# Performance work log

Measured on AMD Instinct MI355X. Metric: run time of the kernel, lower is better.

The kernel has to match this reference:

```python
import jax, jax.numpy as jnp
import numpy as np

B, S, K, N = 4, 2048, 4096, 16384  # batch, seq, in_features, out_features


def setup_inputs() -> dict:
    key = jax.random.key(0)
    k1, k2, k3, k4 = jax.random.split(key, 4)
    x = jax.random.normal(k1, (B, S, K), dtype=jnp.float32)
    # symmetric int8 quantized weights, stored as int32 (values in int8 range)
    W_q = jax.random.randint(k2, (N, K), -128, 128, dtype=jnp.int32)
    # per-output-channel scales (positive, divisor in original code)
    scales = jax.random.uniform(k3, (N,), dtype=jnp.float32, minval=0.5, maxval=2.0)
    bias = jax.random.normal(k4, (N,), dtype=jnp.float32)
    return {"x": x, "W_q": W_q, "scales": scales, "bias": bias}


def reference(x, W_q, scales, bias):
    # out = (x @ W_q.T) / scales + bias   (dequantize-by-division, per out channel)
    Wf = W_q.astype(x.dtype)                       # [N, K]
    lead = x.shape[:-1]
    out = jnp.einsum('tk,nk->tn', x.reshape(-1, x.shape[-1]), Wf)  # [B*S, N]
    out = out / scales[None, :] + bias[None, :]
    return out.reshape(lead + (W_q.shape[0],))
```

## Files before the change

kernel.cpp:

```cpp
#include <hip/hip_runtime.h>
#include <hip/hip_bf16.h>
#include <stdint.h>
#include <stddef.h>

#define M_DIM 8192
#define K_DIM 4096
#define N_DIM 16384

typedef __attribute__((ext_vector_type(8))) short short8;
typedef __attribute__((ext_vector_type(4))) float f32x4;

__device__ __forceinline__ unsigned short f2bf(float f) {
    union { float f; uint32_t u; } c; c.f = f;
    uint32_t u = c.u;
    return (unsigned short)((u + 0x7FFFu + ((u >> 16) & 1u)) >> 16);
}


__global__ __launch_bounds__(256) void conv_x_kernel(const float* __restrict__ x,
                                                     unsigned short* __restrict__ out) {
    size_t i = ((size_t)blockIdx.x * 256 + threadIdx.x) * 8;
    const float4* p = (const float4*)(x + i);
    float4 u = p[0], v = p[1];
    short8 h;
    h[0] = (short)f2bf(u.x); h[1] = (short)f2bf(u.y);
    h[2] = (short)f2bf(u.z); h[3] = (short)f2bf(u.w);
    h[4] = (short)f2bf(v.x); h[5] = (short)f2bf(v.y);
    h[6] = (short)f2bf(v.z); h[7] = (short)f2bf(v.w);
    *(short8*)(out + i) = h;
}

__global__ __launch_bounds__(256) void conv_w_kernel(const int* __restrict__ w,
                                                     unsigned short* __restrict__ out) {
    size_t i = ((size_t)blockIdx.x * 256 + threadIdx.x) * 8;
    const int4* p = (const int4*)(w + i);
    int4 u = p[0], v = p[1];
    short8 h;
    h[0] = (short)f2bf((float)u.x); h[1] = (short)f2bf((float)u.y);
    h[2] = (short)f2bf((float)u.z); h[3] = (short)f2bf((float)u.w);
    h[4] = (short)f2bf((float)v.x); h[5] = (short)f2bf((float)v.y);
    h[6] = (short)f2bf((float)v.z); h[7] = (short)f2bf((float)v.w);
    *(short8*)(out + i) = h;
}


__device__ __forceinline__ void gld_lds16(const void* g, void* l) {
    __builtin_amdgcn_global_load_lds(
        (__attribute__((address_space(1))) void*)(g),
        (__attribute__((address_space(3))) void*)(l),
        16, 0, 0);
}


__global__ __launch_bounds__(256) void gemm_a_kernel(
    const unsigned short* __restrict__ A,
    const unsigned short* __restrict__ Bm,
    const float* __restrict__ scales,
    const float* __restrict__ bias,
    float* __restrict__ C) {
    __shared__ unsigned short As[128 * 64];
    __shared__ unsigned short Bs[128 * 64];

    const int tid = threadIdx.x;
    const int m0 = blockIdx.y * 128;
    const int n0 = blockIdx.x * 128;
    const int lane = tid & 63;
    const int wv = tid >> 6;
    const int wm = (wv & 1) * 64;
    const int wn = (wv >> 1) * 64;
    const int lm = lane & 15;
    const int lk = (lane >> 4) * 8;

    f32x4 acc[4][4] = {};

    for (int kt = 0; kt < K_DIM / 64; ++kt) {
        const int k0 = kt * 64;
#pragma unroll
        for (int i = 0; i < 4; ++i) {
            int c = tid + i * 256;
            int row = c >> 3, col = (c & 7) * 8;
            gld_lds16(A + (size_t)(m0 + row) * K_DIM + k0 + col, (char*)As + c * 16);
        }
#pragma unroll
        for (int i = 0; i < 4; ++i) {
            int c = tid + i * 256;
            int row = c >> 3, col = (c & 7) * 8;
            gld_lds16(Bm + (size_t)(n0 + row) * K_DIM + k0 + col, (char*)Bs + c * 16);
        }
        __syncthreads();

#pragma unroll
        for (int kk = 0; kk < 64; kk += 32) {
            short8 af[4], bfr[4];
#pragma unroll
            for (int im = 0; im < 4; ++im)
                af[im] = *(const short8*)&As[(wm + im * 16 + lm) * 64 + kk + lk];
#pragma unroll
            for (int jn = 0; jn < 4; ++jn)
                bfr[jn] = *(const short8*)&Bs[(wn + jn * 16 + lm) * 64 + kk + lk];
#pragma unroll
            for (int im = 0; im < 4; ++im)
#pragma unroll
                for (int jn = 0; jn < 4; ++jn)
                    acc[im][jn] = __builtin_amdgcn_mfma_f32_16x16x32_bf16(
                        af[im], bfr[jn], acc[im][jn], 0, 0, 0);
        }
        __syncthreads();
    }

#pragma unroll
    for (int jn = 0; jn < 4; ++jn) {
        const int col = n0 + wn + jn * 16 + lm;
        const float inv = 1.0f / scales[col];
        const float bb = bias[col];
#pragma unroll
        for (int im = 0; im < 4; ++im) {
            const int r0 = m0 + wm + im * 16 + (lane >> 4) * 4;
#pragma unroll
            for (int r = 0; r < 4; ++r)
                C[(size_t)(r0 + r) * N_DIM + col] = acc[im][jn][r] * inv + bb;
        }
    }
}


__global__ __launch_bounds__(256) void gemm_b_kernel(
    const float* __restrict__ X,
    const int* __restrict__ W,
    const float* __restrict__ scales,
    const float* __restrict__ bias,
    float* __restrict__ C) {
    __shared__ unsigned short As[128 * 64];
    __shared__ unsigned short Bs[128 * 64];

    const int tid = threadIdx.x;
    const int m0 = blockIdx.y * 128;
    const int n0 = blockIdx.x * 128;
    const int lane = tid & 63;
    const int wv = tid >> 6;
    const int wm = (wv & 1) * 64;
    const int wn = (wv >> 1) * 64;
    const int lm = lane & 15;
    const int lk = (lane >> 4) * 8;

    f32x4 acc[4][4] = {};

    for (int kt = 0; kt < K_DIM / 64; ++kt) {
        const int k0 = kt * 64;
#pragma unroll
        for (int i = 0; i < 4; ++i) {
            int c = tid + i * 256;
            int row = c >> 3, col = (c & 7) * 8;
            const float* p = X + (size_t)(m0 + row) * K_DIM + k0 + col;
            float4 u = *(const float4*)p;
            float4 v = *(const float4*)(p + 4);
            short8 h;
            h[0] = (short)f2bf(u.x); h[1] = (short)f2bf(u.y);
            h[2] = (short)f2bf(u.z); h[3] = (short)f2bf(u.w);
            h[4] = (short)f2bf(v.x); h[5] = (short)f2bf(v.y);
            h[6] = (short)f2bf(v.z); h[7] = (short)f2bf(v.w);
            *(short8*)&As[(size_t)c * 8] = h;
        }
#pragma unroll
        for (int i = 0; i < 4; ++i) {
            int c = tid + i * 256;
            int row = c >> 3, col = (c & 7) * 8;
            const int* p = W + (size_t)(n0 + row) * K_DIM + k0 + col;
            int4 u = *(const int4*)p;
            int4 v = *(const int4*)(p + 4);
            short8 h;
            h[0] = (short)f2bf((float)u.x); h[1] = (short)f2bf((float)u.y);
            h[2] = (short)f2bf((float)u.z); h[3] = (short)f2bf((float)u.w);
            h[4] = (short)f2bf((float)v.x); h[5] = (short)f2bf((float)v.y);
            h[6] = (short)f2bf((float)v.z); h[7] = (short)f2bf((float)v.w);
            *(short8*)&Bs[(size_t)c * 8] = h;
        }
        __syncthreads();

#pragma unroll
        for (int kk = 0; kk < 64; kk += 32) {
            short8 af[4], bfr[4];
#pragma unroll
            for (int im = 0; im < 4; ++im)
                af[im] = *(const short8*)&As[(wm + im * 16 + lm) * 64 + kk + lk];
#pragma unroll
            for (int jn = 0; jn < 4; ++jn)
                bfr[jn] = *(const short8*)&Bs[(wn + jn * 16 + lm) * 64 + kk + lk];
#pragma unroll
            for (int im = 0; im < 4; ++im)
#pragma unroll
                for (int jn = 0; jn < 4; ++jn)
                    acc[im][jn] = __builtin_amdgcn_mfma_f32_16x16x32_bf16(
                        af[im], bfr[jn], acc[im][jn], 0, 0, 0);
        }
        __syncthreads();
    }

#pragma unroll
    for (int jn = 0; jn < 4; ++jn) {
        const int col = n0 + wn + jn * 16 + lm;
        const float inv = 1.0f / scales[col];
        const float bb = bias[col];
#pragma unroll
        for (int im = 0; im < 4; ++im) {
            const int r0 = m0 + wm + im * 16 + (lane >> 4) * 4;
#pragma unroll
            for (int r = 0; r < 4; ++r)
                C[(size_t)(r0 + r) * N_DIM + col] = acc[im][jn][r] * inv + bb;
        }
    }
}


extern "C" void kernel_launch(void* const* d_in, const int* in_sizes, int n_in,
                              void* d_out, int out_size, void* d_ws, size_t ws_size,
                              hipStream_t stream) {
    const float* x      = (const float*)d_in[0];
    const int*   wq     = (const int*)d_in[1];
    const float* scales = (const float*)d_in[2];
    const float* bias   = (const float*)d_in[3];
    float* out = (float*)d_out;

    const size_t x_elems = (size_t)M_DIM * K_DIM;
    const size_t w_elems = (size_t)N_DIM * K_DIM;
    const size_t need = (x_elems + w_elems) * sizeof(unsigned short);

    dim3 grid(N_DIM / 128, M_DIM / 128);

    if (ws_size >= need) {
        unsigned short* xbf = (unsigned short*)d_ws;
        unsigned short* wbf = xbf + x_elems;
        conv_x_kernel<<<(int)(x_elems / (256 * 8)), 256, 0, stream>>>(x, xbf);
        conv_w_kernel<<<(int)(w_elems / (256 * 8)), 256, 0, stream>>>(wq, wbf);
        gemm_a_kernel<<<grid, 256, 0, stream>>>(xbf, wbf, scales, bias, out);
    } else {
        gemm_b_kernel<<<grid, 256, 0, stream>>>(x, wq, scales, bias, out);
    }
}
```

Measured before the change: 2.320 ms.

## Rewrite bf16 GEMM as 256x256 tile, 8-wave, double-buffered pipelined kernel

Replaces the 128x128 single-buffered GEMM with a 256x256-tile, 512-thread kernel. It double-buffers LDS, uses XOR-swizzled layouts to avoid bank conflicts, and interleaves async global-to-LDS loads of the next K tile with four MFMA phases. The phases are separated by barriers and raised wave priority, and tiles are remapped for L2 locality. This targets global-load latency stalls and LDS conflicts. In exchange it needs 128KB of LDS and many accumulator registers, and relies on careful vmcnt accounting that is fragile.

```diff
diff --git a/kernel.cpp b/kernel.cpp
--- a/kernel.cpp
+++ b/kernel.cpp
@@ -6,6 +6,7 @@
 #define M_DIM 8192
 #define K_DIM 4096
 #define N_DIM 16384
+#define NT (K_DIM / 64)
 
 typedef __attribute__((ext_vector_type(8))) short short8;
 typedef __attribute__((ext_vector_type(4))) float f32x4;
@@ -51,74 +52,172 @@
         16, 0, 0);
 }
 
-
-__global__ __launch_bounds__(256) void gemm_a_kernel(
+__device__ __forceinline__ void stage_half(const unsigned short* __restrict__ src,
+                                           unsigned short* lbase, int tid) {
+#pragma unroll
+    for (int i = 0; i < 2; ++i) {
+        int c = tid + i * 512;
+        int row = c >> 3;
+        int col = ((c & 7) ^ (row & 7)) << 3;
+        gld_lds16(src + (size_t)row * K_DIM + col, (char*)lbase + (size_t)c * 16);
+    }
+}
+
+__device__ __forceinline__ short8 lds_frag(const unsigned short* base, int r, int kc) {
+    return *(const short8*)(base + r * 64 + ((kc ^ (r & 7)) << 3));
+}
+
+#define BAR()                                \
+    do {                                     \
+        asm volatile("" ::: "memory");       \
+        __builtin_amdgcn_s_barrier();        \
+        asm volatile("" ::: "memory");       \
+    } while (0)
+#define LGKM0() asm volatile("s_waitcnt lgkmcnt(0)" ::: "memory")
+
+
+__global__ __launch_bounds__(512, 2) void gemm_a_kernel(
     const unsigned short* __restrict__ A,
     const unsigned short* __restrict__ Bm,
     const float* __restrict__ scales,
     const float* __restrict__ bias,
     float* __restrict__ C) {
-    __shared__ unsigned short As[128 * 64];
-    __shared__ unsigned short Bs[128 * 64];
+    __shared__ unsigned short As[2][256 * 64];
+    __shared__ unsigned short Bs[2][256 * 64];
 
     const int tid = threadIdx.x;
-    const int m0 = blockIdx.y * 128;
-    const int n0 = blockIdx.x * 128;
     const int lane = tid & 63;
     const int wv = tid >> 6;
-    const int wm = (wv & 1) * 64;
+    const int wm = (wv & 1) * 128;
     const int wn = (wv >> 1) * 64;
     const int lm = lane & 15;
-    const int lk = (lane >> 4) * 8;
-
-    f32x4 acc[4][4] = {};
-
-    for (int kt = 0; kt < K_DIM / 64; ++kt) {
-        const int k0 = kt * 64;
-#pragma unroll
-        for (int i = 0; i < 4; ++i) {
-            int c = tid + i * 256;
-            int row = c >> 3, col = (c & 7) * 8;
-            gld_lds16(A + (size_t)(m0 + row) * K_DIM + k0 + col, (char*)As + c * 16);
-        }
-#pragma unroll
-        for (int i = 0; i < 4; ++i) {
-            int c = tid + i * 256;
-            int row = c >> 3, col = (c & 7) * 8;
-            gld_lds16(Bm + (size_t)(n0 + row) * K_DIM + k0 + col, (char*)Bs + c * 16);
-        }
-        __syncthreads();
-
-#pragma unroll
-        for (int kk = 0; kk < 64; kk += 32) {
-            short8 af[4], bfr[4];
-#pragma unroll
-            for (int im = 0; im < 4; ++im)
-                af[im] = *(const short8*)&As[(wm + im * 16 + lm) * 64 + kk + lk];
-#pragma unroll
-            for (int jn = 0; jn < 4; ++jn)
-                bfr[jn] = *(const short8*)&Bs[(wn + jn * 16 + lm) * 64 + kk + lk];
-#pragma unroll
-            for (int im = 0; im < 4; ++im)
-#pragma unroll
-                for (int jn = 0; jn < 4; ++jn)
+    const int kseg = lane >> 4;
+
+    const int bid = blockIdx.x;
+    const int tm = (bid & 7) * 4 + ((bid >> 3) & 3);
+    const int tn = bid >> 5;
+    const int m0 = tm * 256, n0 = tn * 256;
+
+    const unsigned short* Ab = A + (size_t)m0 * K_DIM;
+    const unsigned short* Bb = Bm + (size_t)n0 * K_DIM;
+
+    f32x4 acc[8][4] = {};
+    short8 a[4][2], bA[2][2], bB[2][2];
+
+    stage_half(Ab,                            &As[0][0],        tid);
+    stage_half(Ab + (size_t)128 * K_DIM,      &As[0][128 * 64], tid);
+    stage_half(Bb,                            &Bs[0][0],        tid);
+    stage_half(Bb + (size_t)128 * K_DIM,      &Bs[0][128 * 64], tid);
+    stage_half(Bb + 64,                       &Bs[1][0],        tid);
+    stage_half(Bb + (size_t)128 * K_DIM + 64, &Bs[1][128 * 64], tid);
+    asm volatile("s_waitcnt vmcnt(4)" ::: "memory");
+    BAR();
+
+    for (int t = 0; t < NT; ++t) {
+        const int cb = t & 1;
+        const unsigned short* Ac = &As[cb][0];
+        const unsigned short* Bc = &Bs[cb][0];
+        unsigned short* Anx = &As[cb ^ 1][0];
+        unsigned short* Bnx = &Bs[cb][0];
+        const size_t kA = (size_t)((t + 1 < NT) ? t + 1 : NT - 1) * 64;
+        const size_t kB = (size_t)((t + 2 < NT) ? t + 2 : NT - 1) * 64;
+
+#pragma unroll
+        for (int im = 0; im < 4; ++im)
+#pragma unroll
+            for (int kx = 0; kx < 2; ++kx)
+                a[im][kx] = lds_frag(Ac, wm + im * 16 + lm, kx * 4 + kseg);
+#pragma unroll
+        for (int jn = 0; jn < 2; ++jn)
+#pragma unroll
+            for (int kx = 0; kx < 2; ++kx)
+                bA[jn][kx] = lds_frag(Bc, wn + jn * 16 + lm, kx * 4 + kseg);
+        stage_half(Ab + kA, Anx, tid);
+        BAR();
+        LGKM0();
+        __builtin_amdgcn_s_setprio(1);
+#pragma unroll
+        for (int im = 0; im < 4; ++im)
+#pragma unroll
+            for (int jn = 0; jn < 2; ++jn)
+#pragma unroll
+                for (int kx = 0; kx < 2; ++kx)
                     acc[im][jn] = __builtin_amdgcn_mfma_f32_16x16x32_bf16(
-                        af[im], bfr[jn], acc[im][jn], 0, 0, 0);
-        }
-        __syncthreads();
-    }
+                        a[im][kx], bA[jn][kx], acc[im][jn], 0, 0, 0);
+        __builtin_amdgcn_s_setprio(0);
+        BAR();
+
+#pragma unroll
+        for (int jn = 0; jn < 2; ++jn)
+#pragma unroll
+            for (int kx = 0; kx < 2; ++kx)
+                bB[jn][kx] = lds_frag(Bc, wn + (jn + 2) * 16 + lm, kx * 4 + kseg);
+        stage_half(Ab + (size_t)128 * K_DIM + kA, Anx + 128 * 64, tid);
+        BAR();
+        LGKM0();
+        __builtin_amdgcn_s_setprio(1);
+#pragma unroll
+        for (int im = 0; im < 4; ++im)
+#pragma unroll
+            for (int jn = 0; jn < 2; ++jn)
+#pragma unroll
+                for (int kx = 0; kx < 2; ++kx)
+                    acc[im][jn + 2] = __builtin_amdgcn_mfma_f32_16x16x32_bf16(
+                        a[im][kx], bB[jn][kx], acc[im][jn + 2], 0, 0, 0);
+        __builtin_amdgcn_s_setprio(0);
+        BAR();
+
+#pragma unroll
+        for (int im = 0; im < 4; ++im)
+#pragma unroll
+            for (int kx = 0; kx < 2; ++kx)
+                a[im][kx] = lds_frag(Ac, wm + (im + 4) * 16 + lm, kx * 4 + kseg);
+        stage_half(Bb + kB, Bnx, tid);
+        BAR();
+        LGKM0();
+        __builtin_amdgcn_s_setprio(1);
+#pragma unroll
+        for (int im = 0; im < 4; ++im)
+#pragma unroll
+            for (int jn = 0; jn < 2; ++jn)
+#pragma unroll
+                for (int kx = 0; kx < 2; ++kx)
+                    acc[im + 4][jn + 2] = __builtin_amdgcn_mfma_f32_16x16x32_bf16(
+                        a[im][kx], bB[jn][kx], acc[im + 4][jn + 2], 0, 0, 0);
+        __builtin_amdgcn_s_setprio(0);
+        BAR();
+
+        stage_half(Bb + (size_t)128 * K_DIM + kB, Bnx + 128 * 64, tid);
+        BAR();
+        LGKM0();
+        __builtin_amdgcn_s_setprio(1);
+#pragma unroll
+        for (int im = 0; im < 4; ++im)
+#pragma unroll
+            for (int jn = 0; jn < 2; ++jn)
+#pragma unroll
+                for (int kx = 0; kx < 2; ++kx)
+                    acc[im + 4][jn] = __builtin_amdgcn_mfma_f32_16x16x32_bf16(
+                        a[im][kx], bA[jn][kx], acc[im + 4][jn], 0, 0, 0);
+        __builtin_amdgcn_s_setprio(0);
+        asm volatile("s_waitcnt vmcnt(4)" ::: "memory");
+        BAR();
+    }
+
+    asm volatile("s_waitcnt vmcnt(0)" ::: "memory");
+    BAR();
 
 #pragma unroll
     for (int jn = 0; jn < 4; ++jn) {
-        const int col = n0 + wn + jn * 16 + lm;
-        const float inv = 1.0f / scales[col];
-        const float bb = bias[col];
-#pragma unroll
-        for (int im = 0; im < 4; ++im) {
-            const int r0 = m0 + wm + im * 16 + (lane >> 4) * 4;
+        const int coln = n0 + wn + jn * 16 + lm;
+        const float inv = 1.0f / scales[coln];
+        const float bb = bias[coln];
+#pragma unroll
+        for (int im = 0; im < 8; ++im) {
+            const int r0 = m0 + wm + im * 16 + kseg * 4;
 #pragma unroll
             for (int r = 0; r < 4; ++r)
-                C[(size_t)(r0 + r) * N_DIM + col] = acc[im][jn][r] * inv + bb;
+                C[(size_t)(r0 + r) * N_DIM + coln] = acc[im][jn][r] * inv + bb;
         }
     }
 }
@@ -225,15 +324,15 @@
     const size_t w_elems = (size_t)N_DIM * K_DIM;
     const size_t need = (x_elems + w_elems) * sizeof(unsigned short);
 
-    dim3 grid(N_DIM / 128, M_DIM / 128);
-
     if (ws_size >= need) {
         unsigned short* xbf = (unsigned short*)d_ws;
         unsigned short* wbf = xbf + x_elems;
         conv_x_kernel<<<(int)(x_elems / (256 * 8)), 256, 0, stream>>>(x, xbf);
         conv_w_kernel<<<(int)(w_elems / (256 * 8)), 256, 0, stream>>>(wq, wbf);
-        gemm_a_kernel<<<grid, 256, 0, stream>>>(xbf, wbf, scales, bias, out);
+        const int nblocks = (M_DIM / 256) * (N_DIM / 256);
+        gemm_a_kernel<<<nblocks, 512, 0, stream>>>(xbf, wbf, scales, bias, out);
     } else {
+        dim3 grid(N_DIM / 128, M_DIM / 128);
         gemm_b_kernel<<<grid, 256, 0, stream>>>(x, wq, scales, bias, out);
     }
 }
```

New measurement: 2.010 ms. 13.4% less time.
